# Kernel optimization log

Hardware: AMD Instinct MI355X
Metric: run time of the kernel (lower is better)

Reference implementation:

```python
import jax, jax.numpy as jnp
import numpy as np

C = 128      # c_in
H = 4        # no_heads
DH = 32      # c_hidden // no_heads (per-head dim)
INF = 1e9
EPS = 1e-5


def setup_inputs() -> dict:
    key = jax.random.key(0)
    ks = jax.random.split(key, 10)
    B, I, J = 1, 384, 384
    x = jax.random.normal(ks[0], (B, I, J, C), dtype=jnp.float32)
    mask = jnp.ones((B, I, J), dtype=jnp.float32)
    s = 0.02
    return {
        "x": x,
        "mask": mask,
        "ln_w": jnp.ones((C,), jnp.float32),
        "ln_b": jnp.zeros((C,), jnp.float32),
        "w_tri": jax.random.normal(ks[1], (C, H), jnp.float32) * s,   # bias=False
        "wq": jax.random.normal(ks[2], (C, H * DH), jnp.float32) * s,
        "wk": jax.random.normal(ks[3], (C, H * DH), jnp.float32) * s,
        "wv": jax.random.normal(ks[4], (C, H * DH), jnp.float32) * s,
        "wg": jax.random.normal(ks[5], (C, H * DH), jnp.float32) * s,
        "bg": jnp.zeros((H * DH,), jnp.float32),
        "wo": jax.random.normal(ks[6], (H * DH, C), jnp.float32) * s,
        "bo": jnp.zeros((C,), jnp.float32),
    }


def reference(x, mask, ln_w, ln_b, w_tri, wq, wk, wv, wg, bg, wo, bo):
    # starting=True: attend along rows (J axis), no transpose.
    B, I, J, _ = x.shape
    # LayerNorm over channel dim
    mu = jnp.mean(x, axis=-1, keepdims=True)
    var = jnp.mean(jnp.square(x - mu), axis=-1, keepdims=True)
    xn = (x - mu) * jax.lax.rsqrt(var + EPS) * ln_w + ln_b

    # mask bias: [B, I, 1, 1, J]
    mask_bias = (INF * (mask - 1.0))[:, :, None, None, :]
    # triangle bias: linear -> [B, I, J, H] -> permute (2,0,1) -> [B, H, I, J] -> [B, 1, H, I, J]
    tri = jnp.einsum('bijc,ch->bhij', xn, w_tri)[:, None]

    # multi-head attention with gating (OpenFold-style), batch dims (B, I), seq J
    q = jnp.einsum('bijc,cf->bijf', xn, wq).reshape(B, I, J, H, DH)
    k = jnp.einsum('bijc,cf->bijf', xn, wk).reshape(B, I, J, H, DH)
    v = jnp.einsum('bijc,cf->bijf', xn, wv).reshape(B, I, J, H, DH)
    q = q / np.sqrt(DH).astype(np.float32)

    # scores: [B, I, H, Q, K] + mask bias + triangle bias
    scores = jnp.einsum('biqhd,bikhd->bihqk', q, k) + mask_bias + tri
    a = jax.nn.softmax(scores, axis=-1)
    o = jnp.einsum('bihqk,bikhd->biqhd', a, v).reshape(B, I, J, H * DH)

    g = jax.nn.sigmoid(jnp.einsum('bijc,cf->bijf', xn, wg) + bg)
    o = o * g
    out = jnp.einsum('bijf,fc->bijc', o, wo) + bo
    return out
```

## Files before the change

### kernel.cpp

```cpp
#include <hip/hip_runtime.h>
#include <hip/hip_bf16.h>

#define NPOS (384*384)
#define JDIM 384
#define CDIM 128
#define HNUM 4
#define DHD  32

#define LOG2E 1.4426950408889634f

typedef __attribute__((ext_vector_type(8))) short short8;
typedef __attribute__((ext_vector_type(4))) float floatx4;
typedef __attribute__((ext_vector_type(4))) unsigned int uintx4;
typedef unsigned short ushort_t;

#if __has_builtin(__builtin_amdgcn_exp2f)
#define EXP2F(x) __builtin_amdgcn_exp2f(x)
#else
#define EXP2F(x) exp2f(x)
#endif

__device__ __forceinline__ float bf2f(unsigned short u){
  unsigned int x = ((unsigned int)u) << 16;
  return __builtin_bit_cast(float, x);
}
__device__ __forceinline__ unsigned short f2bf(float f){
  unsigned int u = __builtin_bit_cast(unsigned int, f);
  u = u + 0x7FFFu + ((u >> 16) & 1u);
  return (unsigned short)(u >> 16);
}
__device__ __forceinline__ unsigned int cvtpk_bf16(float a, float b){
  unsigned int r;
  asm("v_cvt_pk_bf16_f32 %0, %1, %2" : "=v"(r) : "v"(a), "v"(b));
  return r;
}

__global__ __launch_bounds__(256) void ln_tri_kernel(
    const float* __restrict__ x, const float* __restrict__ lnw,
    const float* __restrict__ lnb, const float* __restrict__ wtri,
    ushort_t* __restrict__ xn, float* __restrict__ trip)
{
  int wave = threadIdx.x >> 6, lane = threadIdx.x & 63;
  int pos = blockIdx.x * 4 + wave;
  const float2 xv = *(const float2*)(x + (size_t)pos*CDIM + lane*2);
  float x0 = xv.x, x1 = xv.y;
  float s = x0 + x1, ss = x0*x0 + x1*x1;
  #pragma unroll
  for (int o = 32; o > 0; o >>= 1){ s += __shfl_xor(s, o); ss += __shfl_xor(ss, o); }
  float mu  = s * (1.0f/128.0f);
  float var = ss * (1.0f/128.0f) - mu*mu;
  float rstd = rsqrtf(var + 1e-5f);
  float2 w2 = *(const float2*)(lnw + lane*2);
  float2 b2 = *(const float2*)(lnb + lane*2);
  float n0 = (x0 - mu)*rstd*w2.x + b2.x;
  float n1 = (x1 - mu)*rstd*w2.y + b2.y;
  ushort2 o2; o2.x = f2bf(n0); o2.y = f2bf(n1);
  *(ushort2*)(xn + (size_t)pos*CDIM + lane*2) = o2;
  float4 wt0 = *(const float4*)(wtri + lane*8);
  float4 wt1 = *(const float4*)(wtri + lane*8 + 4);
  float t0 = n0*wt0.x + n1*wt1.x;
  float t1 = n0*wt0.y + n1*wt1.y;
  float t2 = n0*wt0.z + n1*wt1.z;
  float t3 = n0*wt0.w + n1*wt1.w;
  #pragma unroll
  for (int o = 32; o > 0; o >>= 1){
    t0 += __shfl_xor(t0, o); t1 += __shfl_xor(t1, o);
    t2 += __shfl_xor(t2, o); t3 += __shfl_xor(t3, o);
  }
  if (lane == 0){
    int i = pos / JDIM;
    int j = pos - i*JDIM;
    int tp = (j >> 2)*(JDIM*4) + i*4 + (j & 3);
    trip[0*NPOS + tp] = t0 * LOG2E;
    trip[1*NPOS + tp] = t1 * LOG2E;
    trip[2*NPOS + tp] = t2 * LOG2E;
    trip[3*NPOS + tp] = t3 * LOG2E;
  }
}

__global__ __launch_bounds__(256) void wt_kernel(
    const float* wq, const float* wk, const float* wv,
    const float* wg, const float* wo, ushort_t* __restrict__ wt)
{
  int mat = blockIdx.x >> 6;
  int idx = ((blockIdx.x & 63) << 8) | threadIdx.x;
  const float* src = (mat==0)?wq:(mat==1)?wk:(mat==2)?wv:(mat==3)?wg:wo;
  int f = idx >> 7, c = idx & 127;
  wt[mat*16384 + idx] = f2bf(src[c*128 + f]);
}

__device__ __forceinline__ void gemm_body(
    const ushort_t* __restrict__ A, const ushort_t* __restrict__ W,
    void* __restrict__ outv, const float* __restrict__ bias,
    int mode, int row0, ushort_t* As, ushort_t* Bs)
{
  int t = threadIdx.x;
  #pragma unroll
  for (int i = 0; i < 8; i++){
    int v = t + i*256;
    int row = v >> 4, c8 = v & 15;
    *(short8*)(As + row*144 + c8*8) = *(const short8*)(A + (size_t)(row0+row)*CDIM + c8*8);
    *(short8*)(Bs + row*144 + c8*8) = *(const short8*)(W + v*8);
  }
  __syncthreads();
  int w = t >> 6, lane = t & 63;
  int wm = (w & 1) * 64, wn = (w >> 1) * 64;
  int m = lane & 15, q4 = lane >> 4;
  floatx4 acc[4][4];
  #pragma unroll
  for (int mi = 0; mi < 4; mi++)
    #pragma unroll
    for (int ni = 0; ni < 4; ni++)
      acc[mi][ni] = (floatx4){0.f, 0.f, 0.f, 0.f};
  #pragma unroll
  for (int k0 = 0; k0 < 128; k0 += 32){
    int koff = k0 + q4*8;
    short8 af[4], bf[4];
    #pragma unroll
    for (int mi = 0; mi < 4; mi++) af[mi] = *(const short8*)(As + (wm + mi*16 + m)*144 + koff);
    #pragma unroll
    for (int ni = 0; ni < 4; ni++) bf[ni] = *(const short8*)(Bs + (wn + ni*16 + m)*144 + koff);
    #pragma unroll
    for (int mi = 0; mi < 4; mi++)
      #pragma unroll
      for (int ni = 0; ni < 4; ni++)
        acc[mi][ni] = __builtin_amdgcn_mfma_f32_16x16x32_bf16(af[mi], bf[ni], acc[mi][ni], 0, 0, 0);
  }
  const float scale = 0.17677669529663687f * LOG2E;
  #pragma unroll
  for (int mi = 0; mi < 4; mi++){
    #pragma unroll
    for (int ni = 0; ni < 4; ni++){
      int col = wn + ni*16 + m;
      float bv = (mode >= 2) ? bias[col] : 0.f;
      #pragma unroll
      for (int r = 0; r < 4; r++){
        float val = acc[mi][ni][r];
        if (mode == 1) val *= scale;
        else if (mode == 2) val = 1.f / (1.f + __expf(-(val + bv)));
        else if (mode == 3) val += bv;
        int row = wm + mi*16 + q4*4 + r;
        size_t oidx = (size_t)(row0+row)*CDIM + col;
        if (mode == 3) ((float*)outv)[oidx] = val;
        else           ((ushort_t*)outv)[oidx] = f2bf(val);
      }
    }
  }
}

__global__ __launch_bounds__(256) void proj_gemm_kernel(
    const ushort_t* __restrict__ xn, const ushort_t* __restrict__ wt,
    ushort_t* __restrict__ outb, const float* __restrict__ bg)
{
  __shared__ __align__(16) ushort_t As[128*144];
  __shared__ __align__(16) ushort_t Bs[128*144];
  int proj = blockIdx.y;
  int mode = (proj == 0) ? 1 : (proj == 3) ? 2 : 0;
  gemm_body(xn, wt + proj*16384, outb + (size_t)proj*NPOS*CDIM, bg, mode,
            blockIdx.x * 128, As, Bs);
}

__global__ __launch_bounds__(256) void out_gemm_kernel(
    const ushort_t* __restrict__ og, const ushort_t* __restrict__ wt,
    float* __restrict__ out, const float* __restrict__ bo)
{
  __shared__ __align__(16) ushort_t As[128*144];
  __shared__ __align__(16) ushort_t Bs[128*144];
  gemm_body(og, wt, (void*)out, bo, 3, blockIdx.x * 128, As, Bs);
}

#define KS_STRIDE 36
#define VT_STRIDE 392
__global__ __launch_bounds__(512, 4) void attn_kernel(
    const ushort_t* __restrict__ qb, const ushort_t* __restrict__ kb,
    const ushort_t* __restrict__ vb, const ushort_t* __restrict__ gb,
    const float* __restrict__ mask, const float* __restrict__ trip,
    ushort_t* __restrict__ og)
{
  __shared__ __align__(16) ushort_t Ks[JDIM*KS_STRIDE];
  __shared__ __align__(16) ushort_t Vt[32*VT_STRIDE];
  int i = blockIdx.x, h = blockIdx.y;
  int t = threadIdx.x;
  size_t rbase = (size_t)i * JDIM;

  for (int idx = t; idx < JDIM*4; idx += 512){
    int j = idx >> 2, c8 = idx & 3;
    *(short8*)(Ks + j*KS_STRIDE + c8*8) = *(const short8*)(kb + (rbase + j)*CDIM + h*DHD + c8*8);
    short8 v8 = *(const short8*)(vb + (rbase + j)*CDIM + h*DHD + c8*8);
    int jb = j & 31;
    int jp = (j & ~31) | (((jb >> 2) & 3)*8 + ((jb >> 4) << 2) + (jb & 3));
    #pragma unroll
    for (int e = 0; e < 8; e++) Vt[(c8*8 + e)*VT_STRIDE + jp] = (unsigned short)v8[e];
  }
  __syncthreads();

  int w = t >> 6, lane = t & 63;
  int m = lane & 15, q4 = lane >> 4;
  int wm = w * 48;

  short8 qf[3];
  #pragma unroll
  for (int t6 = 0; t6 < 3; t6++)
    qf[t6] = *(const short8*)(qb + (rbase + wm + t6*16 + m)*CDIM + h*DHD + q4*8);

  floatx4 oacc[3][2];
  float lsum[3];
  #pragma unroll
  for (int t6 = 0; t6 < 3; t6++){
    oacc[t6][0] = (floatx4){0.f,0.f,0.f,0.f};
    oacc[t6][1] = (floatx4){0.f,0.f,0.f,0.f};
    lsum[t6] = 0.f;
  }

  const float* triph = trip + (size_t)h * NPOS;
  const float MC = 1e9f * LOG2E;

  for (int kbk = 0; kbk < 12; kbk++){
    int col0 = kbk * 32;
    short8 kf0 = *(const short8*)(Ks + (col0 + m)*KS_STRIDE + q4*8);
    short8 kf1 = *(const short8*)(Ks + (col0 + 16 + m)*KS_STRIDE + q4*8);
    float4 mk0 = *(const float4*)(mask + rbase + col0 + q4*4);
    float4 mk1 = *(const float4*)(mask + rbase + col0 + 16 + q4*4);
    float mb0[4] = {(mk0.x-1.f)*MC, (mk0.y-1.f)*MC, (mk0.z-1.f)*MC, (mk0.w-1.f)*MC};
    float mb1[4] = {(mk1.x-1.f)*MC, (mk1.y-1.f)*MC, (mk1.z-1.f)*MC, (mk1.w-1.f)*MC};
    short8 vf0 = *(const short8*)(Vt + m*VT_STRIDE + col0 + q4*8);
    short8 vf1 = *(const short8*)(Vt + (16 + m)*VT_STRIDE + col0 + q4*8);

    const float* tb0 = triph + (size_t)(kbk*8 + q4)*(JDIM*4);
    const float* tb1 = triph + (size_t)(kbk*8 + 4 + q4)*(JDIM*4);

    #pragma unroll
    for (int t6 = 0; t6 < 3; t6++){
      int q0t = wm + t6*16;
      float4 tt0 = *(const float4*)(tb0 + (q0t + m)*4);
      float4 tt1 = *(const float4*)(tb1 + (q0t + m)*4);
      floatx4 z0 = (floatx4){tt0.x + mb0[0], tt0.y + mb0[1], tt0.z + mb0[2], tt0.w + mb0[3]};
      floatx4 z1 = (floatx4){tt1.x + mb1[0], tt1.y + mb1[1], tt1.z + mb1[2], tt1.w + mb1[3]};
      floatx4 s0 = __builtin_amdgcn_mfma_f32_16x16x32_bf16(kf0, qf[t6], z0, 0, 0, 0);
      floatx4 s1 = __builtin_amdgcn_mfma_f32_16x16x32_bf16(kf1, qf[t6], z1, 0, 0, 0);
      float p0 = EXP2F(s0[0]), p1 = EXP2F(s0[1]), p2 = EXP2F(s0[2]), p3 = EXP2F(s0[3]);
      float p4 = EXP2F(s1[0]), p5 = EXP2F(s1[1]), p6 = EXP2F(s1[2]), p7 = EXP2F(s1[3]);
      lsum[t6] += ((p0 + p1) + (p2 + p3)) + ((p4 + p5) + (p6 + p7));
      uintx4 pk = (uintx4){cvtpk_bf16(p0, p1), cvtpk_bf16(p2, p3),
                           cvtpk_bf16(p4, p5), cvtpk_bf16(p6, p7)};
      short8 pf = __builtin_bit_cast(short8, pk);
      oacc[t6][0] = __builtin_amdgcn_mfma_f32_16x16x32_bf16(pf, vf0, oacc[t6][0], 0, 0, 0);
      oacc[t6][1] = __builtin_amdgcn_mfma_f32_16x16x32_bf16(pf, vf1, oacc[t6][1], 0, 0, 0);
    }
  }

  float lrec[3];
  #pragma unroll
  for (int t6 = 0; t6 < 3; t6++){
    float l = lsum[t6];
    l += __shfl_xor(l, 16);
    l += __shfl_xor(l, 32);
    lrec[t6] = 1.0f / (l + 1e-30f);
  }

  #pragma unroll
  for (int t6 = 0; t6 < 3; t6++){
    #pragma unroll
    for (int r = 0; r < 4; r++){
      float lrq = __shfl(lrec[t6], (q4 << 2) + r);
      int qrow = wm + t6*16 + q4*4 + r;
      #pragma unroll
      for (int dt = 0; dt < 2; dt++){
        size_t oidx = (rbase + qrow)*CDIM + h*DHD + dt*16 + m;
        float o = oacc[t6][dt][r] * lrq * bf2f(gb[oidx]);
        og[oidx] = f2bf(o);
      }
    }
  }
}

extern "C" void kernel_launch(void* const* d_in, const int* in_sizes, int n_in,
                              void* d_out, int out_size, void* d_ws, size_t ws_size,
                              hipStream_t stream)
{
  const float* x    = (const float*)d_in[0];
  const float* mask = (const float*)d_in[1];
  const float* lnw  = (const float*)d_in[2];
  const float* lnb  = (const float*)d_in[3];
  const float* wtri = (const float*)d_in[4];
  const float* wq   = (const float*)d_in[5];
  const float* wk   = (const float*)d_in[6];
  const float* wv   = (const float*)d_in[7];
  const float* wg   = (const float*)d_in[8];
  const float* bg   = (const float*)d_in[9];
  const float* wo   = (const float*)d_in[10];
  const float* bo   = (const float*)d_in[11];

  char* ws = (char*)d_ws;
  const size_t SZ = (size_t)NPOS * CDIM * 2;
  ushort_t* xn  = (ushort_t*)(ws);
  ushort_t* qb  = (ushort_t*)(ws + 1*SZ);
  ushort_t* kbp = (ushort_t*)(ws + 2*SZ);
  ushort_t* vbp = (ushort_t*)(ws + 3*SZ);
  ushort_t* gbp = (ushort_t*)(ws + 4*SZ);
  ushort_t* og  = (ushort_t*)(ws + 5*SZ);
  ushort_t* wt  = (ushort_t*)(ws + 6*SZ);
  float*    tri = (float*)(ws + 6*SZ + 5*16384*2);

  ln_tri_kernel<<<NPOS/4, 256, 0, stream>>>(x, lnw, lnb, wtri, xn, tri);
  wt_kernel<<<320, 256, 0, stream>>>(wq, wk, wv, wg, wo, wt);
  proj_gemm_kernel<<<dim3(NPOS/128, 4), 256, 0, stream>>>(xn, wt, qb, bg);
  attn_kernel<<<dim3(JDIM, HNUM), 512, 0, stream>>>(qb, kbp, vbp, gbp, mask, tri, og);
  out_gemm_kernel<<<NPOS/128, 256, 0, stream>>>(og, wt + 4*16384, (float*)d_out, bo);
}
```

Before: 338.2 us.

## Reuse staged activation tile across all four projections; read weights from global

The projection GEMM now launches one block per 128-row tile and loops over the four projections (q, k, v, gate). The xn tile is loaded into LDS once and reused four times, where before it was reloaded for each projection. Weight fragments are read straight from global/L2 instead of being staged in LDS, which halves shared memory and adds an occupancy hint of 3 blocks. The risk is longer per-block serial work, fewer blocks in the grid, and weight reads that depend on cache hits.

```diff
diff --git a/kernel.cpp b/kernel.cpp
--- a/kernel.cpp
+++ b/kernel.cpp
@@ -89,18 +89,80 @@
   wt[mat*16384 + idx] = f2bf(src[c*128 + f]);
 }
 
-__device__ __forceinline__ void gemm_body(
-    const ushort_t* __restrict__ A, const ushort_t* __restrict__ W,
-    void* __restrict__ outv, const float* __restrict__ bias,
-    int mode, int row0, ushort_t* As, ushort_t* Bs)
-{
+__global__ __launch_bounds__(256, 3) void proj_gemm_kernel(
+    const ushort_t* __restrict__ xn, const ushort_t* __restrict__ wt,
+    ushort_t* __restrict__ outb, const float* __restrict__ bg)
+{
+  __shared__ __align__(16) ushort_t As[128*144];
   int t = threadIdx.x;
+  int row0 = blockIdx.x * 128;
   #pragma unroll
   for (int i = 0; i < 8; i++){
     int v = t + i*256;
     int row = v >> 4, c8 = v & 15;
-    *(short8*)(As + row*144 + c8*8) = *(const short8*)(A + (size_t)(row0+row)*CDIM + c8*8);
-    *(short8*)(Bs + row*144 + c8*8) = *(const short8*)(W + v*8);
+    *(short8*)(As + row*144 + c8*8) = *(const short8*)(xn + (size_t)(row0+row)*CDIM + c8*8);
+  }
+  __syncthreads();
+  int w = t >> 6, lane = t & 63;
+  int wm = (w & 1) * 64, wn = (w >> 1) * 64;
+  int m = lane & 15, q4 = lane >> 4;
+  const float scale = 0.17677669529663687f * LOG2E;
+
+  #pragma unroll 1
+  for (int proj = 0; proj < 4; proj++){
+    const ushort_t* wp = wt + proj*16384;
+    floatx4 acc[4][4];
+    #pragma unroll
+    for (int mi = 0; mi < 4; mi++)
+      #pragma unroll
+      for (int ni = 0; ni < 4; ni++)
+        acc[mi][ni] = (floatx4){0.f, 0.f, 0.f, 0.f};
+    #pragma unroll
+    for (int ks = 0; ks < 4; ks++){
+      int koff = ks*32 + q4*8;
+      short8 af[4], bf[4];
+      #pragma unroll
+      for (int mi = 0; mi < 4; mi++) af[mi] = *(const short8*)(As + (wm + mi*16 + m)*144 + koff);
+      #pragma unroll
+      for (int ni = 0; ni < 4; ni++) bf[ni] = *(const short8*)(wp + (wn + ni*16 + m)*128 + koff);
+      #pragma unroll
+      for (int mi = 0; mi < 4; mi++)
+        #pragma unroll
+        for (int ni = 0; ni < 4; ni++)
+          acc[mi][ni] = __builtin_amdgcn_mfma_f32_16x16x32_bf16(af[mi], bf[ni], acc[mi][ni], 0, 0, 0);
+    }
+    ushort_t* po = outb + (size_t)proj*NPOS*CDIM;
+    #pragma unroll
+    for (int mi = 0; mi < 4; mi++){
+      #pragma unroll
+      for (int ni = 0; ni < 4; ni++){
+        int col = wn + ni*16 + m;
+        float bv = (proj == 3) ? bg[col] : 0.f;
+        #pragma unroll
+        for (int r = 0; r < 4; r++){
+          float val = acc[mi][ni][r];
+          if (proj == 0) val *= scale;
+          else if (proj == 3) val = 1.f / (1.f + __expf(-(val + bv)));
+          int row = wm + mi*16 + q4*4 + r;
+          po[(size_t)(row0+row)*CDIM + col] = f2bf(val);
+        }
+      }
+    }
+  }
+}
+
+__global__ __launch_bounds__(256, 3) void out_gemm_kernel(
+    const ushort_t* __restrict__ og, const ushort_t* __restrict__ wto,
+    float* __restrict__ out, const float* __restrict__ bo)
+{
+  __shared__ __align__(16) ushort_t As[128*144];
+  int t = threadIdx.x;
+  int row0 = blockIdx.x * 128;
+  #pragma unroll
+  for (int i = 0; i < 8; i++){
+    int v = t + i*256;
+    int row = v >> 4, c8 = v & 15;
+    *(short8*)(As + row*144 + c8*8) = *(const short8*)(og + (size_t)(row0+row)*CDIM + c8*8);
   }
   __syncthreads();
   int w = t >> 6, lane = t & 63;
@@ -113,60 +175,32 @@
     for (int ni = 0; ni < 4; ni++)
       acc[mi][ni] = (floatx4){0.f, 0.f, 0.f, 0.f};
   #pragma unroll
-  for (int k0 = 0; k0 < 128; k0 += 32){
-    int koff = k0 + q4*8;
+  for (int ks = 0; ks < 4; ks++){
+    int koff = ks*32 + q4*8;
     short8 af[4], bf[4];
     #pragma unroll
     for (int mi = 0; mi < 4; mi++) af[mi] = *(const short8*)(As + (wm + mi*16 + m)*144 + koff);
     #pragma unroll
-    for (int ni = 0; ni < 4; ni++) bf[ni] = *(const short8*)(Bs + (wn + ni*16 + m)*144 + koff);
+    for (int ni = 0; ni < 4; ni++) bf[ni] = *(const short8*)(wto + (wn + ni*16 + m)*128 + koff);
     #pragma unroll
     for (int mi = 0; mi < 4; mi++)
       #pragma unroll
       for (int ni = 0; ni < 4; ni++)
         acc[mi][ni] = __builtin_amdgcn_mfma_f32_16x16x32_bf16(af[mi], bf[ni], acc[mi][ni], 0, 0, 0);
   }
-  const float scale = 0.17677669529663687f * LOG2E;
   #pragma unroll
   for (int mi = 0; mi < 4; mi++){
     #pragma unroll
     for (int ni = 0; ni < 4; ni++){
       int col = wn + ni*16 + m;
-      float bv = (mode >= 2) ? bias[col] : 0.f;
+      float bv = bo[col];
       #pragma unroll
       for (int r = 0; r < 4; r++){
-        float val = acc[mi][ni][r];
-        if (mode == 1) val *= scale;
-        else if (mode == 2) val = 1.f / (1.f + __expf(-(val + bv)));
-        else if (mode == 3) val += bv;
         int row = wm + mi*16 + q4*4 + r;
-        size_t oidx = (size_t)(row0+row)*CDIM + col;
-        if (mode == 3) ((float*)outv)[oidx] = val;
-        else           ((ushort_t*)outv)[oidx] = f2bf(val);
+        out[(size_t)(row0+row)*CDIM + col] = acc[mi][ni][r] + bv;
       }
     }
   }
-}
-
-__global__ __launch_bounds__(256) void proj_gemm_kernel(
-    const ushort_t* __restrict__ xn, const ushort_t* __restrict__ wt,
-    ushort_t* __restrict__ outb, const float* __restrict__ bg)
-{
-  __shared__ __align__(16) ushort_t As[128*144];
-  __shared__ __align__(16) ushort_t Bs[128*144];
-  int proj = blockIdx.y;
-  int mode = (proj == 0) ? 1 : (proj == 3) ? 2 : 0;
-  gemm_body(xn, wt + proj*16384, outb + (size_t)proj*NPOS*CDIM, bg, mode,
-            blockIdx.x * 128, As, Bs);
-}
-
-__global__ __launch_bounds__(256) void out_gemm_kernel(
-    const ushort_t* __restrict__ og, const ushort_t* __restrict__ wt,
-    float* __restrict__ out, const float* __restrict__ bo)
-{
-  __shared__ __align__(16) ushort_t As[128*144];
-  __shared__ __align__(16) ushort_t Bs[128*144];
-  gemm_body(og, wt, (void*)out, bo, 3, blockIdx.x * 128, As, Bs);
 }
 
 #define KS_STRIDE 36
@@ -304,7 +338,7 @@
 
   ln_tri_kernel<<<NPOS/4, 256, 0, stream>>>(x, lnw, lnb, wtri, xn, tri);
   wt_kernel<<<320, 256, 0, stream>>>(wq, wk, wv, wg, wo, wt);
-  proj_gemm_kernel<<<dim3(NPOS/128, 4), 256, 0, stream>>>(xn, wt, qb, bg);
+  proj_gemm_kernel<<<NPOS/128, 256, 0, stream>>>(xn, wt, qb, bg);
   attn_kernel<<<dim3(JDIM, HNUM), 512, 0, stream>>>(qb, kbp, vbp, gbp, mask, tri, og);
   out_gemm_kernel<<<NPOS/128, 256, 0, stream>>>(og, wt + 4*16384, (float*)d_out, bo);
 }
```

Result: slower. 418.3 us (+23.7%).
